# Kernel optimization log

Measured on AMD Instinct MI355X. Metric: run time of the kernel, lower is better.

Reference implementation:

```python
import jax, jax.numpy as jnp
import numpy as np

HIDDEN = 512
HEADS = 8
DHEAD = HIDDEN // HEADS  # 64


def setup_inputs() -> dict:
    key = jax.random.key(0)
    ks = jax.random.split(key, 12)
    B, S = 2, 2048
    inp = {
        "q": jax.random.normal(ks[0], (B, S, HIDDEN), dtype=jnp.float32),
        "k": jax.random.normal(ks[1], (B, S, HIDDEN), dtype=jnp.float32),
        "v": jax.random.normal(ks[2], (B, S, HIDDEN), dtype=jnp.float32),
        "mask": jnp.zeros((B, 1, 1, S), dtype=bool),
    }
    scale = 1.0 / np.sqrt(HIDDEN)
    for i, name in enumerate(["Wq", "Wk", "Wv", "Wm"]):
        inp[name] = jax.random.normal(ks[3 + i], (HIDDEN, HIDDEN), dtype=jnp.float32) * scale
    for i, name in enumerate(["bq", "bk", "bv", "bm"]):
        inp[name] = jax.random.normal(ks[7 + i], (HIDDEN,), dtype=jnp.float32) * 0.01
    return inp


def reference(q, k, v, mask, Wq, Wk, Wv, Wm, bq, bk, bv, bm):
    B = q.shape[0]
    # Linear projections (torch Linear: x @ W.T + b)
    qh = (jnp.einsum("bsd,ed->bse", q, Wq) + bq).reshape(B, HEADS, -1, DHEAD)
    kh = (jnp.einsum("bsd,ed->bse", k, Wk) + bk).reshape(B, HEADS, -1, DHEAD)
    vh = (jnp.einsum("bsd,ed->bse", v, Wv) + bv).reshape(B, HEADS, -1, DHEAD)
    # NOTE: the original module reshapes [B,S,512] -> [B,8,S',64] directly
    # (splitting the sequence dim into heads, not the hidden dim); replicated here.
    s = jnp.einsum("bhqd,bhkd->bhqk", qh, kh) / jnp.sqrt(jnp.float32(DHEAD))
    s = jnp.where(mask, jnp.float32(-1e9), s)
    s = jax.nn.softmax(s, axis=-1)
    # dropout is identity in eval mode
    attn = jnp.einsum("bhqk,bhkd->bhqd", s, vh)  # [B,H,S',64]
    attn = attn.transpose(0, 2, 1, 3).reshape(B, -1, HIDDEN)
    return jnp.einsum("bsd,ed->bse", attn, Wm) + bm
```

## Files before the change

### kernel.cpp

```cpp
#include <hip/hip_runtime.h>
#include <hip/hip_bf16.h>
#include <math.h>

typedef float  f32x4 __attribute__((ext_vector_type(4)));
typedef short  s16x8 __attribute__((ext_vector_type(8)));
typedef short  s16x4 __attribute__((ext_vector_type(4)));
typedef unsigned short u16x4 __attribute__((ext_vector_type(4)));

__device__ inline unsigned short bfc(float f){
  __hip_bfloat16 h = __float2bfloat16(f);
  unsigned short u; __builtin_memcpy(&u, &h, 2); return u;
}

__device__ inline f32x4 mfma16(s16x4 a, s16x4 b, f32x4 c){
#if __has_builtin(__builtin_amdgcn_mfma_f32_16x16x16_bf16)
  return __builtin_amdgcn_mfma_f32_16x16x16_bf16(a, b, c, 0, 0, 0);
#elif __has_builtin(__builtin_amdgcn_mfma_f32_16x16x16bf16_1k)
  return __builtin_amdgcn_mfma_f32_16x16x16bf16_1k(a, b, c, 0, 0, 0);
#else
  asm("v_mfma_f32_16x16x16_bf16 %0, %1, %2, %0" : "+v"(c) : "v"(a), "v"(b));
  return c;
#endif
}

__device__ inline void gl_lds16(const unsigned short* g, unsigned short* l){
  __builtin_amdgcn_global_load_lds(
      (const __attribute__((address_space(1))) unsigned int*)g,
      (__attribute__((address_space(3))) unsigned int*)l, 16, 0, 0);
}

__global__ __launch_bounds__(256) void cvt_qkv(const float* __restrict__ q, const float* __restrict__ k,
                                               const float* __restrict__ v, unsigned short* __restrict__ dst){
  int z = blockIdx.y;
  const float* src = z==0 ? q : (z==1 ? k : v);
  unsigned short* d = dst + (size_t)z * 2097152;
  int t = blockIdx.x * 256 + threadIdx.x;
  int r = t >> 6, g = t & 63;
  const float* sp = src + (size_t)r * 512 + g * 8;
  f32x4 a0 = *(const f32x4*)sp;
  f32x4 a1 = *(const f32x4*)(sp + 4);
  s16x8 o = { (short)bfc(a0.x),(short)bfc(a0.y),(short)bfc(a0.z),(short)bfc(a0.w),
              (short)bfc(a1.x),(short)bfc(a1.y),(short)bfc(a1.z),(short)bfc(a1.w) };
  size_t off = ((size_t)(((r>>4)*16 + (g>>2))*64 + (g&3)*16 + (r&15))) * 8;
  *(s16x8*)(d + off) = o;
}

__global__ __launch_bounds__(256) void wcvt(const float* __restrict__ w0, const float* __restrict__ w1,
                                            const float* __restrict__ w2, const float* __restrict__ w3,
                                            const unsigned char* __restrict__ mask,
                                            unsigned short* __restrict__ wb, float* __restrict__ mf){
  int y = blockIdx.y;
  int t = blockIdx.x * 256 + threadIdx.x;
  if (y < 4){
    const float* src = y==0 ? w0 : y==1 ? w1 : y==2 ? w2 : w3;
    int c = t >> 6, g = t & 63;
    const float* sp = src + (size_t)c * 512 + g * 8;
    f32x4 a0 = *(const f32x4*)sp;
    f32x4 a1 = *(const f32x4*)(sp + 4);
    s16x8 o = { (short)bfc(a0.x),(short)bfc(a0.y),(short)bfc(a0.z),(short)bfc(a0.w),
                (short)bfc(a1.x),(short)bfc(a1.y),(short)bfc(a1.z),(short)bfc(a1.w) };
    size_t off = ((size_t)(((c>>4)*16 + (g>>2))*64 + (g&3)*16 + (c&15))) * 8;
    *(s16x8*)(wb + y*262144 + off) = o;
  } else if (t < 4096){
    mf[t] = mask[t] ? -1.442695e9f : 0.0f;
  }
}

__global__ __launch_bounds__(256) void proj_gemm(const unsigned short* __restrict__ Ap,
    const unsigned short* __restrict__ Wp,
    const float* __restrict__ bq, const float* __restrict__ bk, const float* __restrict__ bv,
    unsigned short* __restrict__ pout){
  int z = blockIdx.z;
  const unsigned short* A = Ap + (size_t)z * 2097152;
  const unsigned short* W = Wp + (size_t)z * 262144;
  const float* bias = z==0 ? bq : (z==1 ? bk : bv);
  unsigned short* out = pout + (size_t)z * 2097152;

  int w = threadIdx.x >> 6, lane = threadIdx.x & 63;
  int lr = lane & 15, lg = lane >> 4;
  int rt = blockIdx.x * 4 + w;
  int bn = blockIdx.y;

  f32x4 acc[4] = {};
  const unsigned short* Abase = A + ((size_t)rt*8192 + lane*8);
  const unsigned short* Wbase = W + ((size_t)bn*32768 + lane*8);
#pragma unroll 4
  for (int kc = 0; kc < 16; ++kc){
    s16x8 af = *(const s16x8*)(Abase + kc*512);
#pragma unroll
    for (int n = 0; n < 4; ++n){
      s16x8 bf = *(const s16x8*)(Wbase + ((size_t)n*16 + kc)*512);
      acc[n] = __builtin_amdgcn_mfma_f32_16x16x32_bf16(af, bf, acc[n], 0, 0, 0);
    }
  }
  int orow = rt*16 + lg*4;
#pragma unroll
  for (int n = 0; n < 4; ++n){
    int col = bn*64 + n*16 + lr;
    float bv_ = bias[col];
#pragma unroll
    for (int r = 0; r < 4; ++r)
      out[(size_t)(orow + r)*512 + col] = bfc(acc[n][r] + bv_);
  }
}

__global__ __launch_bounds__(256) void vtrans(const unsigned short* __restrict__ Pv,
                                              unsigned short* __restrict__ Vt){
  int kt = blockIdx.x, bh = blockIdx.y;
  int b = bh >> 3, h = bh & 7;
  __shared__ unsigned short t[64][65];
  const unsigned short* src = Pv + (size_t)(b*2048 + h*256)*512 + kt*4096;
  for (int i = threadIdx.x; i < 4096; i += 256){ int r = i >> 6, c = i & 63; t[r][c] = src[i]; }
  __syncthreads();
  unsigned short* dst = Vt + (size_t)bh*131072 + kt*64;
  for (int i = threadIdx.x; i < 4096; i += 256){ int d = i >> 6, kk = i & 63; dst[(size_t)d*2048 + kk] = t[kk][d]; }
}

__global__ __launch_bounds__(512) void flash(const unsigned short* __restrict__ Pq,
                                             const unsigned short* __restrict__ Pk,
                                             const unsigned short* __restrict__ Vt,
                                             const float* __restrict__ mf,
                                             unsigned short* __restrict__ aout){
  int qt = blockIdx.x;
  int bh = blockIdx.y;
  int b = bh >> 3, h = bh & 7;
  int w = threadIdx.x >> 6;
  int wq = w & 3, wk = w >> 2;
  int lane = threadIdx.x & 63;
  int lr = lane & 15, lg = lane >> 4;

  const unsigned short* Qh  = Pq + (size_t)(b*2048 + h*256)*512;
  const unsigned short* Kh  = Pk + (size_t)(b*2048 + h*256)*512 + (size_t)wk*65536;
  const unsigned short* Vth = Vt + (size_t)bh*131072 + wk*1024;
  const float* mrow = mf + b*2048 + wk*1024;

  __shared__ char smem[65536];
  unsigned short* ktile = (unsigned short*)smem;
  unsigned short* vtile = (unsigned short*)(smem + 32768);
  float* obuf = (float*)smem;
  float* mlb  = (float*)(smem + 16384);

  int lrow = lane >> 3;
  int lcol = ((lane & 7) ^ lrow) * 8;

  int q = qt*64 + wq*16 + lr;
  s16x8 qf0 = *(const s16x8*)(Qh + (size_t)q*64 + lg*8);
  s16x8 qf1 = *(const s16x8*)(Qh + (size_t)q*64 + 32 + lg*8);

  float m2 = -INFINITY, l = 0.f;
  f32x4 accT[4] = {};
  int swz = (lr & 7) * 16;

#define STAGE(dbuf, kk0) { \
    int i0 = 2*wq, i1 = 2*wq + 1; \
    unsigned short* kd = ktile + ((dbuf)*2 + wk)*4096; \
    unsigned short* vd = vtile + ((dbuf)*2 + wk)*4096; \
    gl_lds16(Kh  + (size_t)((kk0) + 8*i0 + lrow)*64 + lcol, kd + i0*512); \
    gl_lds16(Kh  + (size_t)((kk0) + 8*i1 + lrow)*64 + lcol, kd + i1*512); \
    gl_lds16(Vth + (size_t)(8*i0 + lrow)*2048 + (kk0) + lcol, vd + i0*512); \
    gl_lds16(Vth + (size_t)(8*i1 + lrow)*2048 + (kk0) + lcol, vd + i1*512); }

  STAGE(0, 0)
  __syncthreads();
  int cur = 0;

  for (int t = 0; t < 16; ++t){
    int k0 = t * 64;
    if (t < 15) STAGE(cur ^ 1, k0 + 64)

    const char* kb = (const char*)(ktile + (cur*2 + wk)*4096);
    const char* vb = (const char*)(vtile + (cur*2 + wk)*4096);

    float s2[4][4];
    __builtin_amdgcn_s_setprio(1);
#pragma unroll
    for (int n = 0; n < 4; ++n){
      int krow = n*16 + lr;
      s16x8 kf0 = *(const s16x8*)(kb + krow*128 + ((lg*16) ^ swz));
      s16x8 kf1 = *(const s16x8*)(kb + krow*128 + ((64 + lg*16) ^ swz));
      f32x4 a = {};
      a = __builtin_amdgcn_mfma_f32_16x16x32_bf16(kf0, qf0, a, 0, 0, 0);
      a = __builtin_amdgcn_mfma_f32_16x16x32_bf16(kf1, qf1, a, 0, 0, 0);
      f32x4 mv = *(const f32x4*)(mrow + k0 + n*16 + lg*4);
#pragma unroll
      for (int r = 0; r < 4; ++r)
        s2[n][r] = __builtin_fmaf(a[r], 0.18033688f, mv[r]);
    }
    __builtin_amdgcn_s_setprio(0);

    float t0 = fmaxf(fmaxf(s2[0][0], s2[0][1]), fmaxf(s2[0][2], s2[0][3]));
    float t1 = fmaxf(fmaxf(s2[1][0], s2[1][1]), fmaxf(s2[1][2], s2[1][3]));
    float t2 = fmaxf(fmaxf(s2[2][0], s2[2][1]), fmaxf(s2[2][2], s2[2][3]));
    float t3 = fmaxf(fmaxf(s2[3][0], s2[3][1]), fmaxf(s2[3][2], s2[3][3]));
    float rm = fmaxf(fmaxf(t0, t1), fmaxf(t2, t3));
    rm = fmaxf(rm, __shfl_xor(rm, 16));
    rm = fmaxf(rm, __shfl_xor(rm, 32));
    if (!__all(rm <= m2 + 11.54f)){
      float mn = fmaxf(m2, rm);
      float al = __builtin_amdgcn_exp2f(m2 - mn);
      l *= al;
#pragma unroll
      for (int nd = 0; nd < 4; ++nd)
#pragma unroll
        for (int r = 0; r < 4; ++r) accT[nd][r] *= al;
      m2 = mn;
    }
    s16x4 pf[4];
#pragma unroll
    for (int n = 0; n < 4; ++n){
      float p0 = __builtin_amdgcn_exp2f(s2[n][0] - m2);
      float p1 = __builtin_amdgcn_exp2f(s2[n][1] - m2);
      float p2 = __builtin_amdgcn_exp2f(s2[n][2] - m2);
      float p3 = __builtin_amdgcn_exp2f(s2[n][3] - m2);
      l += (p0 + p1) + (p2 + p3);
      pf[n] = (s16x4){ (short)bfc(p0), (short)bfc(p1), (short)bfc(p2), (short)bfc(p3) };
    }
    __builtin_amdgcn_s_setprio(1);
#pragma unroll
    for (int n = 0; n < 4; ++n){
#pragma unroll
      for (int nd = 0; nd < 4; ++nd){
        int vrow = nd*16 + lr;
        s16x4 vf = *(const s16x4*)(vb + vrow*128 + ((n*32 + lg*8) ^ swz));
        accT[nd] = mfma16(vf, pf[n], accT[nd]);
      }
    }
    __builtin_amdgcn_s_setprio(0);

    __syncthreads();
    cur ^= 1;
  }
#undef STAGE

  float lt = l + __shfl_xor(l, 16);
  lt += __shfl_xor(lt, 32);

  if (wk == 1){
    if (lg == 0){ mlb[wq*16 + lr] = m2; mlb[64 + wq*16 + lr] = lt; }
#pragma unroll
    for (int nd = 0; nd < 4; ++nd)
      *(f32x4*)&obuf[((size_t)wq*64 + lane)*16 + nd*4] = accT[nd];
  }
  __syncthreads();
  if (wk == 0){
    float m1 = mlb[wq*16 + lr];
    float l1 = mlb[64 + wq*16 + lr];
    float mM = fmaxf(m2, m1);
    float a0 = __builtin_amdgcn_exp2f(m2 - mM);
    float a1 = __builtin_amdgcn_exp2f(m1 - mM);
    float inv = 1.f / (lt*a0 + l1*a1);
    int rt = (b*2048 + q) >> 4;
#pragma unroll
    for (int nd = 0; nd < 4; ++nd){
      f32x4 o1 = *(const f32x4*)&obuf[((size_t)wq*64 + lane)*16 + nd*4];
      int g = h*8 + nd*2 + (lg >> 1);
      u16x4 ov;
#pragma unroll
      for (int r = 0; r < 4; ++r)
        ov[r] = bfc((accT[nd][r]*a0 + o1[r]*a1) * inv);
      unsigned short* dp = aout + ((size_t)((rt*16 + (g>>2))*64 + (g&3)*16 + lr))*8 + (lg&1)*4;
      *(u16x4*)dp = ov;
    }
  }
}

__global__ __launch_bounds__(256) void gemm_out(const unsigned short* __restrict__ Ap,
                                                const unsigned short* __restrict__ Wp,
                                                const float* __restrict__ bias,
                                                float* __restrict__ out){
  int w = threadIdx.x >> 6, lane = threadIdx.x & 63;
  int lr = lane & 15, lg = lane >> 4;
  int rt = blockIdx.x * 4 + w;
  int bn = blockIdx.y;
  f32x4 acc[4] = {};
  const unsigned short* Abase = Ap + ((size_t)rt*8192 + lane*8);
  const unsigned short* Wbase = Wp + ((size_t)bn*32768 + lane*8);
#pragma unroll 4
  for (int kc = 0; kc < 16; ++kc){
    s16x8 af = *(const s16x8*)(Abase + kc*512);
#pragma unroll
    for (int n = 0; n < 4; ++n){
      s16x8 bf = *(const s16x8*)(Wbase + ((size_t)n*16 + kc)*512);
      acc[n] = __builtin_amdgcn_mfma_f32_16x16x32_bf16(af, bf, acc[n], 0, 0, 0);
    }
  }
  int orow = rt*16 + lg*4;
#pragma unroll
  for (int n = 0; n < 4; ++n){
    int col = bn*64 + n*16 + lr;
    float bv_ = bias[col];
#pragma unroll
    for (int r = 0; r < 4; ++r)
      out[(size_t)(orow + r)*512 + col] = acc[n][r] + bv_;
  }
}

extern "C" void kernel_launch(void* const* d_in, const int* in_sizes, int n_in,
                              void* d_out, int out_size, void* d_ws, size_t ws_size,
                              hipStream_t stream) {
  const float* q  = (const float*)d_in[0];
  const float* k  = (const float*)d_in[1];
  const float* v  = (const float*)d_in[2];
  const unsigned char* mask = (const unsigned char*)d_in[3];
  const float* Wq = (const float*)d_in[4];
  const float* Wk = (const float*)d_in[5];
  const float* Wv = (const float*)d_in[6];
  const float* Wm = (const float*)d_in[7];
  const float* bq = (const float*)d_in[8];
  const float* bk = (const float*)d_in[9];
  const float* bv = (const float*)d_in[10];
  const float* bm = (const float*)d_in[11];

  unsigned short* ws = (unsigned short*)d_ws;
  unsigned short* WP   = ws;
  float*          MF   = (float*)(ws + 1048576);
  unsigned short* AP   = ws + 1056768;
  unsigned short* PQ   = ws + 7348224;
  unsigned short* VT   = ws + 13639680;
  unsigned short* AO   = ws + 15736832;

  cvt_qkv<<<dim3(1024, 3), 256, 0, stream>>>(q, k, v, AP);
  wcvt<<<dim3(128, 5), 256, 0, stream>>>(Wq, Wk, Wv, Wm, mask, WP, MF);
  proj_gemm<<<dim3(64, 8, 3), 256, 0, stream>>>(AP, WP, bq, bk, bv, PQ);
  vtrans<<<dim3(32, 16), 256, 0, stream>>>(PQ + 2*2097152, VT);
  flash<<<dim3(32, 16), 512, 0, stream>>>(PQ, PQ + 2097152, VT, MF, AO);
  gemm_out<<<dim3(64, 8), 256, 0, stream>>>(AO, WP + 3*262144, bm, (float*)d_out);
}
```

Baseline: 84.48 us.

## Merge conversion kernels and give each flash wave two query tiles

Result: no change. 85.49 us (+1.2%).

```diff
diff --git a/kernel.cpp b/kernel.cpp
--- a/kernel.cpp
+++ b/kernel.cpp
@@ -29,38 +29,39 @@
       (__attribute__((address_space(3))) unsigned int*)l, 16, 0, 0);
 }
 
-__global__ __launch_bounds__(256) void cvt_qkv(const float* __restrict__ q, const float* __restrict__ k,
-                                               const float* __restrict__ v, unsigned short* __restrict__ dst){
-  int z = blockIdx.y;
-  const float* src = z==0 ? q : (z==1 ? k : v);
-  unsigned short* d = dst + (size_t)z * 2097152;
-  int t = blockIdx.x * 256 + threadIdx.x;
-  int r = t >> 6, g = t & 63;
-  const float* sp = src + (size_t)r * 512 + g * 8;
-  f32x4 a0 = *(const f32x4*)sp;
-  f32x4 a1 = *(const f32x4*)(sp + 4);
-  s16x8 o = { (short)bfc(a0.x),(short)bfc(a0.y),(short)bfc(a0.z),(short)bfc(a0.w),
-              (short)bfc(a1.x),(short)bfc(a1.y),(short)bfc(a1.z),(short)bfc(a1.w) };
-  size_t off = ((size_t)(((r>>4)*16 + (g>>2))*64 + (g&3)*16 + (r&15))) * 8;
-  *(s16x8*)(d + off) = o;
-}
-
-__global__ __launch_bounds__(256) void wcvt(const float* __restrict__ w0, const float* __restrict__ w1,
+__global__ __launch_bounds__(256) void prep(const float* __restrict__ q, const float* __restrict__ k,
+                                            const float* __restrict__ v,
+                                            const float* __restrict__ w0, const float* __restrict__ w1,
                                             const float* __restrict__ w2, const float* __restrict__ w3,
                                             const unsigned char* __restrict__ mask,
-                                            unsigned short* __restrict__ wb, float* __restrict__ mf){
+                                            unsigned short* __restrict__ AP, unsigned short* __restrict__ WP,
+                                            float* __restrict__ mf){
   int y = blockIdx.y;
   int t = blockIdx.x * 256 + threadIdx.x;
-  if (y < 4){
-    const float* src = y==0 ? w0 : y==1 ? w1 : y==2 ? w2 : w3;
-    int c = t >> 6, g = t & 63;
-    const float* sp = src + (size_t)c * 512 + g * 8;
+  if (y < 3){
+    const float* src = y==0 ? q : (y==1 ? k : v);
+    unsigned short* d = AP + (size_t)y * 2097152;
+    int r = t >> 6, g = t & 63;
+    const float* sp = src + (size_t)r * 512 + g * 8;
     f32x4 a0 = *(const f32x4*)sp;
     f32x4 a1 = *(const f32x4*)(sp + 4);
     s16x8 o = { (short)bfc(a0.x),(short)bfc(a0.y),(short)bfc(a0.z),(short)bfc(a0.w),
                 (short)bfc(a1.x),(short)bfc(a1.y),(short)bfc(a1.z),(short)bfc(a1.w) };
-    size_t off = ((size_t)(((c>>4)*16 + (g>>2))*64 + (g&3)*16 + (c&15))) * 8;
-    *(s16x8*)(wb + y*262144 + off) = o;
+    size_t off = ((size_t)(((r>>4)*16 + (g>>2))*64 + (g&3)*16 + (r&15))) * 8;
+    *(s16x8*)(d + off) = o;
+  } else if (y < 7){
+    if (blockIdx.x < 128){
+      int yy = y - 3;
+      const float* src = yy==0 ? w0 : yy==1 ? w1 : yy==2 ? w2 : w3;
+      int c = t >> 6, g = t & 63;
+      const float* sp = src + (size_t)c * 512 + g * 8;
+      f32x4 a0 = *(const f32x4*)sp;
+      f32x4 a1 = *(const f32x4*)(sp + 4);
+      s16x8 o = { (short)bfc(a0.x),(short)bfc(a0.y),(short)bfc(a0.z),(short)bfc(a0.w),
+                  (short)bfc(a1.x),(short)bfc(a1.y),(short)bfc(a1.z),(short)bfc(a1.w) };
+      size_t off = ((size_t)(((c>>4)*16 + (g>>2))*64 + (g&3)*16 + (c&15))) * 8;
+      *(s16x8*)(WP + yy*262144 + off) = o;
+    }
   } else if (t < 4096){
     mf[t] = mask[t] ? -1.442695e9f : 0.0f;
   }
@@ -116,7 +117,7 @@
   for (int i = threadIdx.x; i < 4096; i += 256){ int d = i >> 6, kk = i & 63; dst[(size_t)d*2048 + kk] = t[kk][d]; }
 }
 
-__global__ __launch_bounds__(512) void flash(const unsigned short* __restrict__ Pq,
+__global__ __launch_bounds__(256) void flash(const unsigned short* __restrict__ Pq,
                                              const unsigned short* __restrict__ Pk,
                                              const unsigned short* __restrict__ Vt,
                                              const float* __restrict__ mf,
@@ -125,7 +126,7 @@
   int bh = blockIdx.y;
   int b = bh >> 3, h = bh & 7;
   int w = threadIdx.x >> 6;
-  int wq = w & 3, wk = w >> 2;
+  int wq = w & 1, wk = w >> 1;
   int lane = threadIdx.x & 63;
   int lr = lane & 15, lg = lane >> 4;
 
@@ -143,22 +144,27 @@
   int lrow = lane >> 3;
   int lcol = ((lane & 7) ^ lrow) * 8;
 
-  int q = qt*64 + wq*16 + lr;
-  s16x8 qf0 = *(const s16x8*)(Qh + (size_t)q*64 + lg*8);
-  s16x8 qf1 = *(const s16x8*)(Qh + (size_t)q*64 + 32 + lg*8);
-
-  float m2 = -INFINITY, l = 0.f;
-  f32x4 accT[4] = {};
+  s16x8 qf[2][2];
+#pragma unroll
+  for (int qq = 0; qq < 2; ++qq){
+    int qrow = qt*64 + wq*32 + qq*16 + lr;
+    qf[qq][0] = *(const s16x8*)(Qh + (size_t)qrow*64 + lg*8);
+    qf[qq][1] = *(const s16x8*)(Qh + (size_t)qrow*64 + 32 + lg*8);
+  }
+
+  float m2[2] = {-INFINITY, -INFINITY}, l[2] = {0.f, 0.f};
+  f32x4 accT[2][4] = {};
   int swz = (lr & 7) * 16;
 
 #define STAGE(dbuf, kk0) { \
-    int i0 = 2*wq, i1 = 2*wq + 1; \
     unsigned short* kd = ktile + ((dbuf)*2 + wk)*4096; \
     unsigned short* vd = vtile + ((dbuf)*2 + wk)*4096; \
-    gl_lds16(Kh  + (size_t)((kk0) + 8*i0 + lrow)*64 + lcol, kd + i0*512); \
-    gl_lds16(Kh  + (size_t)((kk0) + 8*i1 + lrow)*64 + lcol, kd + i1*512); \
-    gl_lds16(Vth + (size_t)(8*i0 + lrow)*2048 + (kk0) + lcol, vd + i0*512); \
-    gl_lds16(Vth + (size_t)(8*i1 + lrow)*2048 + (kk0) + lcol, vd + i1*512); }
+    _Pragma("unroll") \
+    for (int ii = 0; ii < 4; ++ii){ \
+      int i = wq*4 + ii; \
+      gl_lds16(Kh  + (size_t)((kk0) + 8*i + lrow)*64 + lcol, kd + i*512); \
+      gl_lds16(Vth + (size_t)(8*i + lrow)*2048 + (kk0) + lcol, vd + i*512); \
+    } }
 
   STAGE(0, 0)
   __syncthreads();
@@ -171,50 +177,57 @@
     const char* kb = (const char*)(ktile + (cur*2 + wk)*4096);
     const char* vb = (const char*)(vtile + (cur*2 + wk)*4096);
 
-    float s2[4][4];
+    float s2[2][4][4];
     __builtin_amdgcn_s_setprio(1);
 #pragma unroll
     for (int n = 0; n < 4; ++n){
       int krow = n*16 + lr;
       s16x8 kf0 = *(const s16x8*)(kb + krow*128 + ((lg*16) ^ swz));
       s16x8 kf1 = *(const s16x8*)(kb + krow*128 + ((64 + lg*16) ^ swz));
-      f32x4 a = {};
-      a = __builtin_amdgcn_mfma_f32_16x16x32_bf16(kf0, qf0, a, 0, 0, 0);
-      a = __builtin_amdgcn_mfma_f32_16x16x32_bf16(kf1, qf1, a, 0, 0, 0);
       f32x4 mv = *(const f32x4*)(mrow + k0 + n*16 + lg*4);
 #pragma unroll
-      for (int r = 0; r < 4; ++r)
-        s2[n][r] = __builtin_fmaf(a[r], 0.18033688f, mv[r]);
+      for (int qq = 0; qq < 2; ++qq){
+        f32x4 a = {};
+        a = __builtin_amdgcn_mfma_f32_16x16x32_bf16(kf0, qf[qq][0], a, 0, 0, 0);
+        a = __builtin_amdgcn_mfma_f32_16x16x32_bf16(kf1, qf[qq][1], a, 0, 0, 0);
+#pragma unroll
+        for (int r = 0; r < 4; ++r)
+          s2[qq][n][r] = __builtin_fmaf(a[r], 0.18033688f, mv[r]);
+      }
     }
     __builtin_amdgcn_s_setprio(0);
 
-    float t0 = fmaxf(fmaxf(s2[0][0], s2[0][1]), fmaxf(s2[0][2], s2[0][3]));
-    float t1 = fmaxf(fmaxf(s2[1][0], s2[1][1]), fmaxf(s2[1][2], s2[1][3]));
-    float t2 = fmaxf(fmaxf(s2[2][0], s2[2][1]), fmaxf(s2[2][2], s2[2][3]));
-    float t3 = fmaxf(fmaxf(s2[3][0], s2[3][1]), fmaxf(s2[3][2], s2[3][3]));
-    float rm = fmaxf(fmaxf(t0, t1), fmaxf(t2, t3));
-    rm = fmaxf(rm, __shfl_xor(rm, 16));
-    rm = fmaxf(rm, __shfl_xor(rm, 32));
-    if (!__all(rm <= m2 + 11.54f)){
-      float mn = fmaxf(m2, rm);
-      float al = __builtin_amdgcn_exp2f(m2 - mn);
-      l *= al;
-#pragma unroll
-      for (int nd = 0; nd < 4; ++nd)
-#pragma unroll
-        for (int r = 0; r < 4; ++r) accT[nd][r] *= al;
-      m2 = mn;
-    }
-    s16x4 pf[4];
-#pragma unroll
-    for (int n = 0; n < 4; ++n){
-      float p0 = __builtin_amdgcn_exp2f(s2[n][0] - m2);
-      float p1 = __builtin_amdgcn_exp2f(s2[n][1] - m2);
-      float p2 = __builtin_amdgcn_exp2f(s2[n][2] - m2);
-      float p3 = __builtin_amdgcn_exp2f(s2[n][3] - m2);
-      l += (p0 + p1) + (p2 + p3);
-      pf[n] = (s16x4){ (short)bfc(p0), (short)bfc(p1), (short)bfc(p2), (short)bfc(p3) };
-    }
+    s16x4 pf[2][4];
+#pragma unroll
+    for (int qq = 0; qq < 2; ++qq){
+      float t0 = fmaxf(fmaxf(s2[qq][0][0], s2[qq][0][1]), fmaxf(s2[qq][0][2], s2[qq][0][3]));
+      float t1 = fmaxf(fmaxf(s2[qq][1][0], s2[qq][1][1]), fmaxf(s2[qq][1][2], s2[qq][1][3]));
+      float t2 = fmaxf(fmaxf(s2[qq][2][0], s2[qq][2][1]), fmaxf(s2[qq][2][2], s2[qq][2][3]));
+      float t3 = fmaxf(fmaxf(s2[qq][3][0], s2[qq][3][1]), fmaxf(s2[qq][3][2], s2[qq][3][3]));
+      float rm = fmaxf(fmaxf(t0, t1), fmaxf(t2, t3));
+      rm = fmaxf(rm, __shfl_xor(rm, 16));
+      rm = fmaxf(rm, __shfl_xor(rm, 32));
+      if (!__all(rm <= m2[qq] + 11.54f)){
+        float mn = fmaxf(m2[qq], rm);
+        float al = __builtin_amdgcn_exp2f(m2[qq] - mn);
+        l[qq] *= al;
+#pragma unroll
+        for (int nd = 0; nd < 4; ++nd)
+#pragma unroll
+          for (int r = 0; r < 4; ++r) accT[qq][nd][r] *= al;
+        m2[qq] = mn;
+      }
+#pragma unroll
+      for (int n = 0; n < 4; ++n){
+        float p0 = __builtin_amdgcn_exp2f(s2[qq][n][0] - m2[qq]);
+        float p1 = __builtin_amdgcn_exp2f(s2[qq][n][1] - m2[qq]);
+        float p2 = __builtin_amdgcn_exp2f(s2[qq][n][2] - m2[qq]);
+        float p3 = __builtin_amdgcn_exp2f(s2[qq][n][3] - m2[qq]);
+        l[qq] += (p0 + p1) + (p2 + p3);
+        pf[qq][n] = (s16x4){ (short)bfc(p0), (short)bfc(p1), (short)bfc(p2), (short)bfc(p3) };
+      }
+    }
+
     __builtin_amdgcn_s_setprio(1);
 #pragma unroll
     for (int n = 0; n < 4; ++n){
@@ -222,7 +235,8 @@
       for (int nd = 0; nd < 4; ++nd){
         int vrow = nd*16 + lr;
         s16x4 vf = *(const s16x4*)(vb + vrow*128 + ((n*32 + lg*8) ^ swz));
-        accT[nd] = mfma16(vf, pf[n], accT[nd]);
+        accT[0][nd] = mfma16(vf, pf[0][n], accT[0][nd]);
+        accT[1][nd] = mfma16(vf, pf[1][n], accT[1][nd]);
       }
     }
     __builtin_amdgcn_s_setprio(0);
@@ -232,34 +246,47 @@
   }
 #undef STAGE
 
-  float lt = l + __shfl_xor(l, 16);
-  lt += __shfl_xor(lt, 32);
+  float lt[2];
+#pragma unroll
+  for (int qq = 0; qq < 2; ++qq){
+    float x = l[qq] + __shfl_xor(l[qq], 16);
+    lt[qq] = x + __shfl_xor(x, 32);
+  }
 
   if (wk == 1){
-    if (lg == 0){ mlb[wq*16 + lr] = m2; mlb[64 + wq*16 + lr] = lt; }
-#pragma unroll
-    for (int nd = 0; nd < 4; ++nd)
-      *(f32x4*)&obuf[((size_t)wq*64 + lane)*16 + nd*4] = accT[nd];
+#pragma unroll
+    for (int qq = 0; qq < 2; ++qq){
+      int wb2 = wq*2 + qq;
+      if (lg == 0){ mlb[wb2*16 + lr] = m2[qq]; mlb[64 + wb2*16 + lr] = lt[qq]; }
+#pragma unroll
+      for (int nd = 0; nd < 4; ++nd)
+        *(f32x4*)&obuf[((size_t)wb2*64 + lane)*16 + nd*4] = accT[qq][nd];
+    }
   }
   __syncthreads();
   if (wk == 0){
-    float m1 = mlb[wq*16 + lr];
-    float l1 = mlb[64 + wq*16 + lr];
-    float mM = fmaxf(m2, m1);
-    float a0 = __builtin_amdgcn_exp2f(m2 - mM);
-    float a1 = __builtin_amdgcn_exp2f(m1 - mM);
-    float inv = 1.f / (lt*a0 + l1*a1);
-    int rt = (b*2048 + q) >> 4;
-#pragma unroll
-    for (int nd = 0; nd < 4; ++nd){
-      f32x4 o1 = *(const f32x4*)&obuf[((size_t)wq*64 + lane)*16 + nd*4];
-      int g = h*8 + nd*2 + (lg >> 1);
-      u16x4 ov;
-#pragma unroll
-      for (int r = 0; r < 4; ++r)
-        ov[r] = bfc((accT[nd][r]*a0 + o1[r]*a1) * inv);
-      unsigned short* dp = aout + ((size_t)((rt*16 + (g>>2))*64 + (g&3)*16 + lr))*8 + (lg&1)*4;
-      *(u16x4*)dp = ov;
+#pragma unroll
+    for (int qq = 0; qq < 2; ++qq){
+      int wb2 = wq*2 + qq;
+      float m1 = mlb[wb2*16 + lr];
+      float l1 = mlb[64 + wb2*16 + lr];
+      float mM = fmaxf(m2[qq], m1);
+      float a0 = __builtin_amdgcn_exp2f(m2[qq] - mM);
+      float a1 = __builtin_amdgcn_exp2f(m1 - mM);
+      float inv = 1.f / (lt[qq]*a0 + l1*a1);
+      int q = qt*64 + wq*32 + qq*16 + lr;
+      int rt = (b*2048 + q) >> 4;
+#pragma unroll
+      for (int nd = 0; nd < 4; ++nd){
+        f32x4 o1 = *(const f32x4*)&obuf[((size_t)wb2*64 + lane)*16 + nd*4];
+        int g = h*8 + nd*2 + (lg >> 1);
+        u16x4 ov;
+#pragma unroll
+        for (int r = 0; r < 4; ++r)
+          ov[r] = bfc((accT[qq][nd][r]*a0 + o1[r]*a1) * inv);
+        unsigned short* dp = aout + ((size_t)((rt*16 + (g>>2))*64 + (g&3)*16 + lr))*8 + (lg&1)*4;
+        *(u16x4*)dp = ov;
+      }
     }
   }
 }
@@ -319,10 +346,9 @@
   unsigned short* VT   = ws + 13639680;
   unsigned short* AO   = ws + 15736832;
 
-  cvt_qkv<<<dim3(1024, 3), 256, 0, stream>>>(q, k, v, AP);
-  wcvt<<<dim3(128, 5), 256, 0, stream>>>(Wq, Wk, Wv, Wm, mask, WP, MF);
+  prep<<<dim3(1024, 8), 256, 0, stream>>>(q, k, v, Wq, Wk, Wv, Wm, mask, AP, WP, MF);
   proj_gemm<<<dim3(64, 8, 3), 256, 0, stream>>>(AP, WP, bq, bk, bv, PQ);
   vtrans<<<dim3(32, 16), 256, 0, stream>>>(PQ + 2*2097152, VT);
-  flash<<<dim3(32, 16), 512, 0, stream>>>(PQ, PQ + 2097152, VT, MF, AO);
+  flash<<<dim3(32, 16), 256, 0, stream>>>(PQ, PQ + 2097152, VT, MF, AO);
   gemm_out<<<dim3(64, 8), 256, 0, stream>>>(AO, WP + 3*262144, bm, (float*)d_out);
 }
```
